# Optimization experiments

Hardware: AMD Instinct MI355X
Metric: run time of the kernel (lower is better)

The kernel has to match this reference:

```python
import jax, jax.numpy as jnp
import numpy as np
from jax import lax

SMOOTHING = 0.3
B, T, D = 64, 4096, 256


def setup_inputs() -> dict:
    key = jax.random.key(0)
    x = jax.random.normal(key, (B, T, D), dtype=jnp.float32)
    return {"x": x}


def reference(x) -> jnp.ndarray:
    # EMA linear recurrence: y[0] = x[0]; y[t] = s*x[t] + (1-s)*y[t-1]
    # Expressed as y[t] = a[t]*y[t-1] + b[t] and solved with an associative scan.
    s = jnp.asarray(SMOOTHING, x.dtype)
    t = x.shape[1]
    # a: (1, T, 1) broadcastable coefficient; a[0]=0 so y[0]=b[0]=x[0]
    a = jnp.full((1, t, 1), 1.0 - s, dtype=x.dtype).at[:, 0].set(0.0)
    b = (s * x).at[:, 0].set(x[:, 0])

    def combine(c1, c2):
        a1, b1 = c1
        a2, b2 = c2
        return a1 * a2, a2 * b1 + b2

    _, y = lax.associative_scan(combine, (a, b), axis=1)
    return y
```

## Files before the change

### kernel.cpp

```cpp
#include <hip/hip_runtime.h>


constexpr int   Bc = 64;
constexpr int   Tc = 4096;
constexpr int   Dc = 256;
constexpr float S  = 0.3f;
constexpr float R  = 1.0f - S;

constexpr int L  = 256;
constexpr int W  = 32;
constexpr int DP = Dc / 2;
constexpr int NC = Tc / L;

__global__ __launch_bounds__(256)
void ema_f32_kernel(const float2* __restrict__ x,
                    float2* __restrict__ y)
{
    const int tid = blockIdx.x * 256 + threadIdx.x;
    const int dp  = tid & (DP - 1);
    const int c   = (tid >> 7) & (NC - 1);
    const int b   = tid >> 11;
    const int t0  = c * L;
    const long base = (long)b * Tc * DP + dp;

    float y0 = 0.0f, y1 = 0.0f;
    int tstart = t0;

    if (c == 0) {
        float2 v = x[base];
        y0 = v.x;
        y1 = v.y;
        y[base] = v;
        tstart = 1;
    } else {
        #pragma unroll
        for (int t = t0 - W; t < t0; ++t) {
            float2 v = x[base + (long)t * DP];
            y0 = fmaf(R, y0, S * v.x);
            y1 = fmaf(R, y1, S * v.y);
        }
    }

    #pragma unroll 8
    for (int t = tstart; t < t0 + L; ++t) {
        float2 v = x[base + (long)t * DP];
        y0 = fmaf(R, y0, S * v.x);
        y1 = fmaf(R, y1, S * v.y);
        float2 o;
        o.x = y0;
        o.y = y1;
        y[base + (long)t * DP] = o;
    }
}

extern "C" void kernel_launch(void* const* d_in, const int* in_sizes, int n_in,
                              void* d_out, int out_size, void* d_ws, size_t ws_size,
                              hipStream_t stream) {
    (void)in_sizes; (void)n_in; (void)d_ws; (void)ws_size; (void)out_size;
    const float2* x = (const float2*)d_in[0];
    float2*       y = (float2*)d_out;

    const int total_threads = Bc * NC * DP;
    dim3 grid(total_threads / 256), block(256);
    hipLaunchKernelGGL(ema_f32_kernel, grid, block, 0, stream, x, y);
}
```

Baseline: 443.4 us.

## Vectorize EMA to float4, halve chunk length, swizzle blocks, nontemporal stores

Each thread now handles four channels with 16-byte loads and stores instead of two with 8-byte accesses, and the chunk length drops from 256 to 128 so the grid stays the same size. Block indices are permuted across groups of eight, likely to spread work across XCDs, and outputs are written with nontemporal stores to avoid polluting cache. The shorter chunk means the 32-step warmup rereads a larger fraction of the input, and offsets switch to 32-bit int arithmetic.

```diff
diff --git a/kernel.cpp b/kernel.cpp
--- a/kernel.cpp
+++ b/kernel.cpp
@@ -1,5 +1,7 @@
 #include <hip/hip_runtime.h>
 
+
+typedef float f32x4 __attribute__((ext_vector_type(4)));
 
 constexpr int   Bc = 64;
 constexpr int   Tc = 4096;
@@ -7,49 +9,54 @@
 constexpr float S  = 0.3f;
 constexpr float R  = 1.0f - S;
 
-constexpr int L  = 256;
+constexpr int L  = 128;
 constexpr int W  = 32;
-constexpr int DP = Dc / 2;
+constexpr int DQ = Dc / 4;
 constexpr int NC = Tc / L;
 
 __global__ __launch_bounds__(256)
-void ema_f32_kernel(const float2* __restrict__ x,
-                    float2* __restrict__ y)
+void ema_f32_kernel(const f32x4* __restrict__ x,
+                    f32x4* __restrict__ y)
 {
-    const int tid = blockIdx.x * 256 + threadIdx.x;
-    const int dp  = tid & (DP - 1);
-    const int c   = (tid >> 7) & (NC - 1);
+    const int cpx = gridDim.x >> 3;
+    const int lb  = (blockIdx.x & 7) * cpx + (blockIdx.x >> 3);
+
+    const int tid = lb * 256 + (int)threadIdx.x;
+    const int dq  = tid & (DQ - 1);
+    const int c   = (tid >> 6) & (NC - 1);
     const int b   = tid >> 11;
     const int t0  = c * L;
-    const long base = (long)b * Tc * DP + dp;
+    const int base = b * (Tc * DQ) + dq;
 
-    float y0 = 0.0f, y1 = 0.0f;
+    float y0 = 0.f, y1 = 0.f, y2 = 0.f, y3 = 0.f;
     int tstart = t0;
 
     if (c == 0) {
-        float2 v = x[base];
-        y0 = v.x;
-        y1 = v.y;
-        y[base] = v;
+        f32x4 v = x[base];
+        y0 = v.x; y1 = v.y; y2 = v.z; y3 = v.w;
+        __builtin_nontemporal_store(v, &y[base]);
         tstart = 1;
     } else {
-        #pragma unroll
+        #pragma unroll 8
         for (int t = t0 - W; t < t0; ++t) {
-            float2 v = x[base + (long)t * DP];
+            f32x4 v = x[base + t * DQ];
             y0 = fmaf(R, y0, S * v.x);
             y1 = fmaf(R, y1, S * v.y);
+            y2 = fmaf(R, y2, S * v.z);
+            y3 = fmaf(R, y3, S * v.w);
         }
     }
 
     #pragma unroll 8
     for (int t = tstart; t < t0 + L; ++t) {
-        float2 v = x[base + (long)t * DP];
+        f32x4 v = x[base + t * DQ];
         y0 = fmaf(R, y0, S * v.x);
         y1 = fmaf(R, y1, S * v.y);
-        float2 o;
-        o.x = y0;
-        o.y = y1;
-        y[base + (long)t * DP] = o;
+        y2 = fmaf(R, y2, S * v.z);
+        y3 = fmaf(R, y3, S * v.w);
+        f32x4 o;
+        o.x = y0; o.y = y1; o.z = y2; o.w = y3;
+        __builtin_nontemporal_store(o, &y[base + t * DQ]);
     }
 }
 
@@ -57,10 +64,10 @@
                               void* d_out, int out_size, void* d_ws, size_t ws_size,
                               hipStream_t stream) {
     (void)in_sizes; (void)n_in; (void)d_ws; (void)ws_size; (void)out_size;
-    const float2* x = (const float2*)d_in[0];
-    float2*       y = (float2*)d_out;
+    const f32x4* x = (const f32x4*)d_in[0];
+    f32x4*       y = (f32x4*)d_out;
 
-    const int total_threads = Bc * NC * DP;
+    const int total_threads = Bc * NC * DQ;
     dim3 grid(total_threads / 256), block(256);
     hipLaunchKernelGGL(ema_f32_kernel, grid, block, 0, stream, x, y);
 }
```

Result: slower. 452.9 us (+2.1%).
